# Kernel optimization log

Measured on AMD Instinct MI355X. Metric: run time of the kernel, lower is better.

The kernel has to match this reference:

```python
import jax, jax.numpy as jnp
import numpy as np

N = 50000      # nodes
E = 500000     # edges
F_IN = 128     # num_features
H = 128        # hidden_dim
G = 256        # graphs in batch


def setup_inputs() -> dict:
    key = jax.random.key(0)
    ks = jax.random.split(key, 12)
    x = jax.random.normal(ks[0], (N, F_IN), jnp.float32)
    edge_index = jax.random.randint(ks[1], (2, E), 0, N, dtype=jnp.int32)
    edge_attr = jax.random.uniform(ks[2], (E,), jnp.float32)  # positive edge weights
    batch = jnp.sort(jax.random.randint(ks[3], (N,), 0, G, dtype=jnp.int32))
    s_in = 1.0 / np.sqrt(F_IN)
    s_h = 1.0 / np.sqrt(H)
    return {
        "x": x,
        "edge_index": edge_index,
        "edge_attr": edge_attr,
        "batch": batch,
        "W1": jax.random.normal(ks[4], (H, F_IN), jnp.float32) * s_in,
        "b1": jnp.zeros((H,), jnp.float32),
        "W2": jax.random.normal(ks[5], (H, H), jnp.float32) * s_h,
        "b2": jnp.zeros((H,), jnp.float32),
        "fW1": jax.random.normal(ks[6], (H, H), jnp.float32) * s_h,
        "fb1": jnp.zeros((H,), jnp.float32),
        "fW2": jax.random.normal(ks[7], (1, H), jnp.float32) * s_h,
        "fb2": jnp.zeros((1,), jnp.float32),
    }


def gcn_conv(x, src, dst, ew, W, b, n):
    """PyG GCNConv: linear transform, add self-loops (weight 1),
    symmetric deg^-1/2 normalization with edge weights, scatter-add, bias."""
    h = x @ W.T                                   # [n, H]
    loop = jnp.arange(n, dtype=src.dtype)
    s = jnp.concatenate([src, loop])
    d = jnp.concatenate([dst, loop])
    w = jnp.concatenate([ew, jnp.ones((n,), x.dtype)])
    deg = jax.ops.segment_sum(w, d, num_segments=n)  # weighted in-degree incl. self-loop
    dinv = jnp.where(deg > 0, jax.lax.rsqrt(deg), 0.0)
    norm = dinv[s] * w * dinv[d]                  # [E+n]
    msg = h[s] * norm[:, None]                    # gather + scale: [E+n, H]
    out = jax.ops.segment_sum(msg, d, num_segments=n)  # scatter-add
    return out + b


def reference(x, edge_index, edge_attr, batch, W1, b1, W2, b2, fW1, fb1, fW2, fb2):
    src, dst = edge_index[0], edge_index[1]
    h = jax.nn.relu(gcn_conv(x, src, dst, edge_attr, W1, b1, N))
    h = jax.nn.relu(gcn_conv(h, src, dst, edge_attr, W2, b2, N))
    # global_mean_pool over graph ids
    sums = jax.ops.segment_sum(h, batch, num_segments=G)            # [G, H]
    counts = jax.ops.segment_sum(jnp.ones((N,), h.dtype), batch, num_segments=G)
    pooled = sums / jnp.maximum(counts, 1.0)[:, None]
    o = jax.nn.relu(pooled @ fW1.T + fb1)
    return o @ fW2.T + fb2                                          # [G, 1]
```

## Files before the change

### kernel.cpp

```cpp
#include <hip/hip_runtime.h>
#include <hip/hip_bf16.h>


#define CAP 16
#define NREP 4
#define STRIDE 64

typedef __attribute__((ext_vector_type(8))) short short8;
typedef __attribute__((ext_vector_type(4))) float floatx4;

__device__ inline unsigned short f2bf(float f) {
    unsigned int u = __float_as_uint(f);
    u += 0x7FFF + ((u >> 16) & 1);
    return (unsigned short)(u >> 16);
}
__device__ inline float bf2f(unsigned short h) {
    return __uint_as_float(((unsigned int)h) << 16);
}

__global__ void build_csr(const int* __restrict__ src, const int* __restrict__ dst,
                          const float* __restrict__ ew,
                          int* __restrict__ cnt, int2* __restrict__ csr, int e, int n) {
    int i = blockIdx.x * blockDim.x + threadIdx.x;
    if (i < e) {
        int d = dst[i];
        int r = i & (NREP - 1);
        int pos = atomicAdd(&cnt[(size_t)r * n + d], 1);
        csr[((size_t)d << 6) + (r << 4) + pos] = make_int2(src[i], __float_as_int(ew[i]));
    }
}

__global__ __launch_bounds__(256) void deg_from_csr(const int* __restrict__ cnt,
        const int2* __restrict__ csr, float* __restrict__ dinv, int n) {
    int node = blockIdx.x * 8 + (threadIdx.x >> 5);
    int lane = threadIdx.x & 31;
    float s = 0.0f;
    if (node < n) {
        int pos = lane & 15;
        int sa = lane >> 4;
        int sb = 2 + (lane >> 4);
        int ca = cnt[(size_t)sa * n + node];
        int cb = cnt[(size_t)sb * n + node];
        const int2* b = csr + ((size_t)node << 6);
        if (pos < ca) s += __int_as_float(b[lane].y);
        if (pos < cb) s += __int_as_float(b[32 + lane].y);
    }
#pragma unroll
    for (int off = 16; off > 0; off >>= 1) s += __shfl_down(s, off, 32);
    if (node < n && lane == 0) dinv[node] = rsqrtf(s + 1.0f);
}

__global__ __launch_bounds__(256) void fold_compact(int* __restrict__ cnt,
        int2* __restrict__ csr, const float* __restrict__ dinv, int n) {
    int node = blockIdx.x * 8 + (threadIdx.x >> 5);
    if (node >= n) return;
    int lane = threadIdx.x & 31;
    int c0 = cnt[node];
    int c1 = cnt[(size_t)1 * n + node];
    int c2 = cnt[(size_t)2 * n + node];
    int c3 = cnt[(size_t)3 * n + node];
    int pre[4] = {0, c0, c0 + c1, c0 + c1 + c2};
    int cs[4] = {c0, c1, c2, c3};

    int2* b = csr + ((size_t)node << 6);
    int pos = lane & 15;
    int sa = lane >> 4;
    int sb = 2 + (lane >> 4);
    bool va = pos < cs[sa];
    bool vb = pos < cs[sb];
    int2 ea = va ? b[lane] : make_int2(0, 0);
    int2 eb = vb ? b[32 + lane] : make_int2(0, 0);
    if (va) ea.y = __float_as_int(__int_as_float(ea.y) * dinv[ea.x]);
    if (vb) eb.y = __float_as_int(__int_as_float(eb.y) * dinv[eb.x]);
    if (va) b[pre[sa] + pos] = ea;
    if (vb) b[pre[sb] + pos] = eb;
    if (lane == 0) cnt[node] = c0 + c1 + c2 + c3;
}

#define PW 136
__global__ __launch_bounds__(256) void gemm_f32_nt(const float* __restrict__ X,
        const float* __restrict__ W, unsigned short* __restrict__ C, int M) {
    __shared__ unsigned short whi[128 * PW];
    __shared__ unsigned short wlo[128 * PW];
    const int t = threadIdx.x;

    {
        int j = t >> 1;
        int c0 = (t & 1) * 64;
        const floatx4* wr = (const floatx4*)(W + (size_t)j * 128 + c0);
        unsigned short* dh = &whi[j * PW + c0];
        unsigned short* dl = &wlo[j * PW + c0];
#pragma unroll
        for (int i = 0; i < 16; ++i) {
            floatx4 v = wr[i];
            ushort4 hv, lv;
            hv.x = f2bf(v.x); lv.x = f2bf(v.x - bf2f(hv.x));
            hv.y = f2bf(v.y); lv.y = f2bf(v.y - bf2f(hv.y));
            hv.z = f2bf(v.z); lv.z = f2bf(v.z - bf2f(hv.z));
            hv.w = f2bf(v.w); lv.w = f2bf(v.w - bf2f(hv.w));
            *(ushort4*)(dh + i * 4) = hv;
            *(ushort4*)(dl + i * 4) = lv;
        }
    }
    __syncthreads();

    const int wave = t >> 6;
    const int lane = t & 63;
    const int q = lane >> 4;
    const int ln = lane & 15;
    const int rowbase = blockIdx.x * 128 + wave * 32;

    floatx4 acc[2][8];
#pragma unroll
    for (int s = 0; s < 2; ++s)
#pragma unroll
        for (int ct = 0; ct < 8; ++ct) acc[s][ct] = (floatx4){0.f, 0.f, 0.f, 0.f};

#pragma unroll
    for (int ks = 0; ks < 4; ++ks) {
        short8 ahi[2], alo[2];
#pragma unroll
        for (int s = 0; s < 2; ++s) {
            int row = rowbase + s * 16 + ln;
            int rowc = (row < M) ? row : (M - 1);
            const floatx4* xr = (const floatx4*)(X + (size_t)rowc * 128 + ks * 32 + q * 8);
            floatx4 x0 = xr[0];
            floatx4 x1 = xr[1];
            unsigned short h, l;
            h = f2bf(x0.x); l = f2bf(x0.x - bf2f(h)); ahi[s][0] = (short)h; alo[s][0] = (short)l;
            h = f2bf(x0.y); l = f2bf(x0.y - bf2f(h)); ahi[s][1] = (short)h; alo[s][1] = (short)l;
            h = f2bf(x0.z); l = f2bf(x0.z - bf2f(h)); ahi[s][2] = (short)h; alo[s][2] = (short)l;
            h = f2bf(x0.w); l = f2bf(x0.w - bf2f(h)); ahi[s][3] = (short)h; alo[s][3] = (short)l;
            h = f2bf(x1.x); l = f2bf(x1.x - bf2f(h)); ahi[s][4] = (short)h; alo[s][4] = (short)l;
            h = f2bf(x1.y); l = f2bf(x1.y - bf2f(h)); ahi[s][5] = (short)h; alo[s][5] = (short)l;
            h = f2bf(x1.z); l = f2bf(x1.z - bf2f(h)); ahi[s][6] = (short)h; alo[s][6] = (short)l;
            h = f2bf(x1.w); l = f2bf(x1.w - bf2f(h)); ahi[s][7] = (short)h; alo[s][7] = (short)l;
        }
#pragma unroll
        for (int ct = 0; ct < 8; ++ct) {
            int lidx = (ct * 16 + ln) * PW + ks * 32 + q * 8;
            short8 bhi = *(const short8*)&whi[lidx];
            short8 blo = *(const short8*)&wlo[lidx];
#pragma unroll
            for (int s = 0; s < 2; ++s) {
                acc[s][ct] = __builtin_amdgcn_mfma_f32_16x16x32_bf16(ahi[s], bhi, acc[s][ct], 0, 0, 0);
                acc[s][ct] = __builtin_amdgcn_mfma_f32_16x16x32_bf16(ahi[s], blo, acc[s][ct], 0, 0, 0);
                acc[s][ct] = __builtin_amdgcn_mfma_f32_16x16x32_bf16(alo[s], bhi, acc[s][ct], 0, 0, 0);
            }
        }
    }

#pragma unroll
    for (int s = 0; s < 2; ++s) {
#pragma unroll
        for (int r = 0; r < 4; ++r) {
            int row = rowbase + s * 16 + q * 4 + r;
            if (row < M) {
                unsigned short* cr = C + (size_t)row * 128 + ln;
#pragma unroll
                for (int ct = 0; ct < 8; ++ct) cr[ct * 16] = f2bf(acc[s][ct][r]);
            }
        }
    }
}

__global__ __launch_bounds__(256) void gemm_bf16_nt(const unsigned short* __restrict__ X,
        const float* __restrict__ W, unsigned short* __restrict__ C, int M) {
    __shared__ unsigned short whi[128 * PW];
    __shared__ unsigned short wlo[128 * PW];
    const int t = threadIdx.x;

    {
        int j = t >> 1;
        int c0 = (t & 1) * 64;
        const floatx4* wr = (const floatx4*)(W + (size_t)j * 128 + c0);
        unsigned short* dh = &whi[j * PW + c0];
        unsigned short* dl = &wlo[j * PW + c0];
#pragma unroll
        for (int i = 0; i < 16; ++i) {
            floatx4 v = wr[i];
            ushort4 hv, lv;
            hv.x = f2bf(v.x); lv.x = f2bf(v.x - bf2f(hv.x));
            hv.y = f2bf(v.y); lv.y = f2bf(v.y - bf2f(hv.y));
            hv.z = f2bf(v.z); lv.z = f2bf(v.z - bf2f(hv.z));
            hv.w = f2bf(v.w); lv.w = f2bf(v.w - bf2f(hv.w));
            *(ushort4*)(dh + i * 4) = hv;
            *(ushort4*)(dl + i * 4) = lv;
        }
    }
    __syncthreads();

    const int wave = t >> 6;
    const int lane = t & 63;
    const int q = lane >> 4;
    const int ln = lane & 15;
    const int rowbase = blockIdx.x * 128 + wave * 32;

    floatx4 acc[2][8];
#pragma unroll
    for (int s = 0; s < 2; ++s)
#pragma unroll
        for (int ct = 0; ct < 8; ++ct) acc[s][ct] = (floatx4){0.f, 0.f, 0.f, 0.f};

#pragma unroll
    for (int ks = 0; ks < 4; ++ks) {
        short8 a[2];
#pragma unroll
        for (int s = 0; s < 2; ++s) {
            int row = rowbase + s * 16 + ln;
            int rowc = (row < M) ? row : (M - 1);
            a[s] = *(const short8*)(X + (size_t)rowc * 128 + ks * 32 + q * 8);
        }
#pragma unroll
        for (int ct = 0; ct < 8; ++ct) {
            int lidx = (ct * 16 + ln) * PW + ks * 32 + q * 8;
            short8 bhi = *(const short8*)&whi[lidx];
            short8 blo = *(const short8*)&wlo[lidx];
#pragma unroll
            for (int s = 0; s < 2; ++s) {
                acc[s][ct] = __builtin_amdgcn_mfma_f32_16x16x32_bf16(a[s], bhi, acc[s][ct], 0, 0, 0);
                acc[s][ct] = __builtin_amdgcn_mfma_f32_16x16x32_bf16(a[s], blo, acc[s][ct], 0, 0, 0);
            }
        }
    }

#pragma unroll
    for (int s = 0; s < 2; ++s) {
#pragma unroll
        for (int r = 0; r < 4; ++r) {
            int row = rowbase + s * 16 + q * 4 + r;
            if (row < M) {
                unsigned short* cr = C + (size_t)row * 128 + ln;
#pragma unroll
                for (int ct = 0; ct < 8; ++ct) cr[ct * 16] = f2bf(acc[s][ct][r]);
            }
        }
    }
}

__global__ __launch_bounds__(256) void aggregate_finalize(
        const unsigned short* __restrict__ h, const unsigned short* __restrict__ hlin,
        const int* __restrict__ cnt, const int2* __restrict__ csr,
        const float* __restrict__ dinv, const float* __restrict__ bias,
        unsigned short* __restrict__ outb, int n) {
    int node = blockIdx.x * 8 + (threadIdx.x >> 5);
    if (node >= n) return;
    int lane = threadIdx.x & 31;
    float di = dinv[node];
    float sl = di * di;
    float4 b4 = ((const float4*)bias)[lane];
    ushort4 bse = ((const ushort4*)(hlin + (size_t)node * 128))[lane];
    float4 acc = make_float4(0.f, 0.f, 0.f, 0.f);

    const int2* b = csr + ((size_t)node << 6);
    const int4* bv = (const int4*)b;
    int c = cnt[node];
    int k = 0;
    for (; k + 4 <= c; k += 4) {
        int4 ea = bv[k >> 1];
        int4 eb = bv[(k >> 1) + 1];
        float w0 = __int_as_float(ea.y);
        float w1 = __int_as_float(ea.w);
        float w2 = __int_as_float(eb.y);
        float w3 = __int_as_float(eb.w);
        ushort4 h0 = ((const ushort4*)(h + (size_t)ea.x * 128))[lane];
        ushort4 h1 = ((const ushort4*)(h + (size_t)ea.z * 128))[lane];
        ushort4 h2 = ((const ushort4*)(h + (size_t)eb.x * 128))[lane];
        ushort4 h3 = ((const ushort4*)(h + (size_t)eb.z * 128))[lane];
        acc.x += bf2f(h0.x) * w0 + bf2f(h1.x) * w1 + bf2f(h2.x) * w2 + bf2f(h3.x) * w3;
        acc.y += bf2f(h0.y) * w0 + bf2f(h1.y) * w1 + bf2f(h2.y) * w2 + bf2f(h3.y) * w3;
        acc.z += bf2f(h0.z) * w0 + bf2f(h1.z) * w1 + bf2f(h2.z) * w2 + bf2f(h3.z) * w3;
        acc.w += bf2f(h0.w) * w0 + bf2f(h1.w) * w1 + bf2f(h2.w) * w2 + bf2f(h3.w) * w3;
    }
    if (k + 2 <= c) {
        int4 ea = bv[k >> 1];
        float w0 = __int_as_float(ea.y);
        float w1 = __int_as_float(ea.w);
        ushort4 h0 = ((const ushort4*)(h + (size_t)ea.x * 128))[lane];
        ushort4 h1 = ((const ushort4*)(h + (size_t)ea.z * 128))[lane];
        acc.x += bf2f(h0.x) * w0 + bf2f(h1.x) * w1;
        acc.y += bf2f(h0.y) * w0 + bf2f(h1.y) * w1;
        acc.z += bf2f(h0.z) * w0 + bf2f(h1.z) * w1;
        acc.w += bf2f(h0.w) * w0 + bf2f(h1.w) * w1;
        k += 2;
    }
    if (k < c) {
        int2 ed = b[k];
        float w = __int_as_float(ed.y);
        ushort4 hv = ((const ushort4*)(h + (size_t)ed.x * 128))[lane];
        acc.x += bf2f(hv.x) * w;
        acc.y += bf2f(hv.y) * w;
        acc.z += bf2f(hv.z) * w;
        acc.w += bf2f(hv.w) * w;
    }
    ushort4 o;
    o.x = f2bf(fmaxf(acc.x * di + bf2f(bse.x) * sl + b4.x, 0.0f));
    o.y = f2bf(fmaxf(acc.y * di + bf2f(bse.y) * sl + b4.y, 0.0f));
    o.z = f2bf(fmaxf(acc.z * di + bf2f(bse.z) * sl + b4.z, 0.0f));
    o.w = f2bf(fmaxf(acc.w * di + bf2f(bse.w) * sl + b4.w, 0.0f));
    ((ushort4*)(outb + (size_t)node * 128))[lane] = o;
}

#define POOL_BLOCKS 1024
__global__ __launch_bounds__(128) void pool_partial(const unsigned short* __restrict__ h,
        const int* __restrict__ batch, float* __restrict__ pooled, int n) {
    int chunk = (n + POOL_BLOCKS - 1) / POOL_BLOCKS;
    int s = blockIdx.x * chunk;
    if (s >= n) return;
    int e = min(s + chunk, n);
    int j = threadIdx.x;
    int curg = batch[s];
    float sum = 0.0f;
    for (int i = s; i < e; ++i) {
        int g = batch[i];
        if (g != curg) {
            atomicAdd(&pooled[(size_t)curg * 128 + j], sum);
            sum = 0.0f;
            curg = g;
        }
        sum += bf2f(h[(size_t)i * 128 + j]);
    }
    atomicAdd(&pooled[(size_t)curg * 128 + j], sum);
}

__global__ __launch_bounds__(128) void head_mlp(const float* __restrict__ pooled,
        const int* __restrict__ batch, int n,
        const float* __restrict__ fW1, const float* __restrict__ fb1,
        const float* __restrict__ fW2, const float* __restrict__ fb2,
        float* __restrict__ out) {
    int g = blockIdx.x;
    int j = threadIdx.x;
    int lo = 0, hi = n;
    while (lo < hi) { int mid = (lo + hi) >> 1; if (batch[mid] < g) lo = mid + 1; else hi = mid; }
    int s = lo;
    hi = n;
    while (lo < hi) { int mid = (lo + hi) >> 1; if (batch[mid] < g + 1) lo = mid + 1; else hi = mid; }
    int cnt = lo - s;
    float scale = 1.0f / fmaxf((float)cnt, 1.0f);

    __shared__ float row[128];
    __shared__ float part[2];
    row[j] = pooled[(size_t)g * 128 + j] * scale;
    __syncthreads();
    float acc = fb1[j];
    const float* wr = fW1 + (size_t)j * 128;
#pragma unroll 8
    for (int k = 0; k < 128; ++k) acc += row[k] * wr[k];
    float v = fmaxf(acc, 0.0f) * fW2[j];
#pragma unroll
    for (int off = 32; off > 0; off >>= 1) v += __shfl_down(v, off);
    if ((j & 63) == 0) part[j >> 6] = v;
    __syncthreads();
    if (j == 0) out[g] = part[0] + part[1] + fb2[0];
}

extern "C" void kernel_launch(void* const* d_in, const int* in_sizes, int n_in,
                              void* d_out, int out_size, void* d_ws, size_t ws_size,
                              hipStream_t stream) {
    const float* x   = (const float*)d_in[0];
    const int*   ei  = (const int*)d_in[1];
    const float* ew  = (const float*)d_in[2];
    const int* batch = (const int*)d_in[3];
    const float* W1  = (const float*)d_in[4];
    const float* b1  = (const float*)d_in[5];
    const float* W2  = (const float*)d_in[6];
    const float* b2  = (const float*)d_in[7];
    const float* fW1 = (const float*)d_in[8];
    const float* fb1 = (const float*)d_in[9];
    const float* fW2 = (const float*)d_in[10];
    const float* fb2 = (const float*)d_in[11];
    float* out = (float*)d_out;

    const int N = in_sizes[0] / 128;
    const int E = in_sizes[2];
    const int G = out_size;
    const int* src = ei;
    const int* dst = ei + E;

    unsigned short* A = (unsigned short*)d_ws;
    unsigned short* B = A + (size_t)N * 128;
    int2*  csr  = (int2*)(B + (size_t)N * 128);
    int*   cnt  = (int*)(csr + (size_t)N * STRIDE);
    float* dinv = (float*)(cnt + (size_t)NREP * N);
    float* pooled = dinv + N;

    hipMemsetAsync(cnt, 0, (size_t)NREP * N * sizeof(int), stream);
    build_csr<<<(E + 255) / 256, 256, 0, stream>>>(src, dst, ew, cnt, csr, E, N);
    deg_from_csr<<<(N + 7) / 8, 256, 0, stream>>>(cnt, csr, dinv, N);
    fold_compact<<<(N + 7) / 8, 256, 0, stream>>>(cnt, csr, dinv, N);

    gemm_f32_nt<<<(N + 127) / 128, 256, 0, stream>>>(x, W1, A, N);
    aggregate_finalize<<<(N + 7) / 8, 256, 0, stream>>>(A, A, cnt, csr, dinv, b1, B, N);

    gemm_bf16_nt<<<(N + 127) / 128, 256, 0, stream>>>(B, W2, A, N);
    aggregate_finalize<<<(N + 7) / 8, 256, 0, stream>>>(A, A, cnt, csr, dinv, b2, B, N);

    hipMemsetAsync(pooled, 0, (size_t)G * 128 * sizeof(float), stream);
    pool_partial<<<POOL_BLOCKS, 128, 0, stream>>>(B, batch, pooled, N);
    head_mlp<<<G, 128, 0, stream>>>(pooled, batch, N, fW1, fb1, fW2, fb2, out);
}
```

Baseline: 237.8 us.

## Fuse degree into CSR build, dinv into GEMM, pooling into final aggregate

CSR construction now uses a single per-node counter with a cap of 64 and accumulates weighted degree with float atomics in the same pass. This removes the deg_from_csr and fold_compact kernels. dinv is computed at the start of the first GEMM kernel, and the source-side dinv multiply moves into the aggregation loops as an extra gathered load per edge. The second aggregation is fused with mean-pool partial sums through shared-memory per-block reduction, which drops the bf16 intermediate write, the pool kernel and one memset. The costs are more atomic contention on the single counter, extra dinv gathers, and silent truncation of any node with more than 64 in-edges.

```diff
diff --git a/kernel.cpp b/kernel.cpp
--- a/kernel.cpp
+++ b/kernel.cpp
@@ -2,9 +2,7 @@
 #include <hip/hip_bf16.h>
 
 
-#define CAP 16
-#define NREP 4
-#define STRIDE 64
+#define CAP 64
 
 typedef __attribute__((ext_vector_type(8))) short short8;
 typedef __attribute__((ext_vector_type(4))) float floatx4;
@@ -20,66 +18,28 @@
 
 __global__ void build_csr(const int* __restrict__ src, const int* __restrict__ dst,
                           const float* __restrict__ ew,
-                          int* __restrict__ cnt, int2* __restrict__ csr, int e, int n) {
+                          int* __restrict__ cnt, float* __restrict__ deg,
+                          int2* __restrict__ csr, int e, int n) {
     int i = blockIdx.x * blockDim.x + threadIdx.x;
     if (i < e) {
         int d = dst[i];
-        int r = i & (NREP - 1);
-        int pos = atomicAdd(&cnt[(size_t)r * n + d], 1);
-        csr[((size_t)d << 6) + (r << 4) + pos] = make_int2(src[i], __float_as_int(ew[i]));
-    }
-}
-
-__global__ __launch_bounds__(256) void deg_from_csr(const int* __restrict__ cnt,
-        const int2* __restrict__ csr, float* __restrict__ dinv, int n) {
-    int node = blockIdx.x * 8 + (threadIdx.x >> 5);
-    int lane = threadIdx.x & 31;
-    float s = 0.0f;
-    if (node < n) {
-        int pos = lane & 15;
-        int sa = lane >> 4;
-        int sb = 2 + (lane >> 4);
-        int ca = cnt[(size_t)sa * n + node];
-        int cb = cnt[(size_t)sb * n + node];
-        const int2* b = csr + ((size_t)node << 6);
-        if (pos < ca) s += __int_as_float(b[lane].y);
-        if (pos < cb) s += __int_as_float(b[32 + lane].y);
-    }
-#pragma unroll
-    for (int off = 16; off > 0; off >>= 1) s += __shfl_down(s, off, 32);
-    if (node < n && lane == 0) dinv[node] = rsqrtf(s + 1.0f);
-}
-
-__global__ __launch_bounds__(256) void fold_compact(int* __restrict__ cnt,
-        int2* __restrict__ csr, const float* __restrict__ dinv, int n) {
-    int node = blockIdx.x * 8 + (threadIdx.x >> 5);
-    if (node >= n) return;
-    int lane = threadIdx.x & 31;
-    int c0 = cnt[node];
-    int c1 = cnt[(size_t)1 * n + node];
-    int c2 = cnt[(size_t)2 * n + node];
-    int c3 = cnt[(size_t)3 * n + node];
-    int pre[4] = {0, c0, c0 + c1, c0 + c1 + c2};
-    int cs[4] = {c0, c1, c2, c3};
-
-    int2* b = csr + ((size_t)node << 6);
-    int pos = lane & 15;
-    int sa = lane >> 4;
-    int sb = 2 + (lane >> 4);
-    bool va = pos < cs[sa];
-    bool vb = pos < cs[sb];
-    int2 ea = va ? b[lane] : make_int2(0, 0);
-    int2 eb = vb ? b[32 + lane] : make_int2(0, 0);
-    if (va) ea.y = __float_as_int(__int_as_float(ea.y) * dinv[ea.x]);
-    if (vb) eb.y = __float_as_int(__int_as_float(eb.y) * dinv[eb.x]);
-    if (va) b[pre[sa] + pos] = ea;
-    if (vb) b[pre[sb] + pos] = eb;
-    if (lane == 0) cnt[node] = c0 + c1 + c2 + c3;
+        float w = ew[i];
+        int pos = atomicAdd(&cnt[d], 1);
+        if (pos < CAP)
+            csr[((size_t)d << 6) + pos] = make_int2(src[i], __float_as_int(w));
+        atomicAdd(&deg[d], w);
+    }
 }
 
 #define PW 136
 __global__ __launch_bounds__(256) void gemm_f32_nt(const float* __restrict__ X,
-        const float* __restrict__ W, unsigned short* __restrict__ C, int M) {
+        const float* __restrict__ W, unsigned short* __restrict__ C,
+        const float* __restrict__ deg, float* __restrict__ dinv, int M) {
+    {
+        int gid = blockIdx.x * 256 + threadIdx.x;
+        if (gid < M) dinv[gid] = rsqrtf(deg[gid] + 1.0f);
+    }
+
     __shared__ unsigned short whi[128 * PW];
     __shared__ unsigned short wlo[128 * PW];
     const int t = threadIdx.x;
@@ -255,14 +215,15 @@
     const int2* b = csr + ((size_t)node << 6);
     const int4* bv = (const int4*)b;
     int c = cnt[node];
+    if (c > CAP) c = CAP;
     int k = 0;
     for (; k + 4 <= c; k += 4) {
         int4 ea = bv[k >> 1];
         int4 eb = bv[(k >> 1) + 1];
-        float w0 = __int_as_float(ea.y);
-        float w1 = __int_as_float(ea.w);
-        float w2 = __int_as_float(eb.y);
-        float w3 = __int_as_float(eb.w);
+        float w0 = __int_as_float(ea.y) * dinv[ea.x];
+        float w1 = __int_as_float(ea.w) * dinv[ea.z];
+        float w2 = __int_as_float(eb.y) * dinv[eb.x];
+        float w3 = __int_as_float(eb.w) * dinv[eb.z];
         ushort4 h0 = ((const ushort4*)(h + (size_t)ea.x * 128))[lane];
         ushort4 h1 = ((const ushort4*)(h + (size_t)ea.z * 128))[lane];
         ushort4 h2 = ((const ushort4*)(h + (size_t)eb.x * 128))[lane];
@@ -274,8 +235,8 @@
     }
     if (k + 2 <= c) {
         int4 ea = bv[k >> 1];
-        float w0 = __int_as_float(ea.y);
-        float w1 = __int_as_float(ea.w);
+        float w0 = __int_as_float(ea.y) * dinv[ea.x];
+        float w1 = __int_as_float(ea.w) * dinv[ea.z];
         ushort4 h0 = ((const ushort4*)(h + (size_t)ea.x * 128))[lane];
         ushort4 h1 = ((const ushort4*)(h + (size_t)ea.z * 128))[lane];
         acc.x += bf2f(h0.x) * w0 + bf2f(h1.x) * w1;
@@ -286,7 +247,7 @@
     }
     if (k < c) {
         int2 ed = b[k];
-        float w = __int_as_float(ed.y);
+        float w = __int_as_float(ed.y) * dinv[ed.x];
         ushort4 hv = ((const ushort4*)(h + (size_t)ed.x * 128))[lane];
         acc.x += bf2f(hv.x) * w;
         acc.y += bf2f(hv.y) * w;
@@ -301,26 +262,94 @@
     ((ushort4*)(outb + (size_t)node * 128))[lane] = o;
 }
 
-#define POOL_BLOCKS 1024
-__global__ __launch_bounds__(128) void pool_partial(const unsigned short* __restrict__ h,
+__global__ __launch_bounds__(256) void aggregate_pool(
+        const unsigned short* __restrict__ h,
+        const int* __restrict__ cnt, const int2* __restrict__ csr,
+        const float* __restrict__ dinv, const float* __restrict__ bias,
         const int* __restrict__ batch, float* __restrict__ pooled, int n) {
-    int chunk = (n + POOL_BLOCKS - 1) / POOL_BLOCKS;
-    int s = blockIdx.x * chunk;
-    if (s >= n) return;
-    int e = min(s + chunk, n);
-    int j = threadIdx.x;
-    int curg = batch[s];
-    float sum = 0.0f;
-    for (int i = s; i < e; ++i) {
-        int g = batch[i];
-        if (g != curg) {
-            atomicAdd(&pooled[(size_t)curg * 128 + j], sum);
-            sum = 0.0f;
-            curg = g;
-        }
-        sum += bf2f(h[(size_t)i * 128 + j]);
-    }
-    atomicAdd(&pooled[(size_t)curg * 128 + j], sum);
+    int slot = threadIdx.x >> 5;
+    int node = blockIdx.x * 8 + slot;
+    int lane = threadIdx.x & 31;
+    __shared__ float red[8][128];
+    __shared__ int grp[8];
+
+    float4 o = make_float4(0.f, 0.f, 0.f, 0.f);
+    int g = -1;
+    if (node < n) {
+        g = batch[node];
+        float di = dinv[node];
+        float sl = di * di;
+        float4 b4 = ((const float4*)bias)[lane];
+        ushort4 bse = ((const ushort4*)(h + (size_t)node * 128))[lane];
+        float4 acc = make_float4(0.f, 0.f, 0.f, 0.f);
+
+        const int2* b = csr + ((size_t)node << 6);
+        const int4* bv = (const int4*)b;
+        int c = cnt[node];
+        if (c > CAP) c = CAP;
+        int k = 0;
+        for (; k + 4 <= c; k += 4) {
+            int4 ea = bv[k >> 1];
+            int4 eb = bv[(k >> 1) + 1];
+            float w0 = __int_as_float(ea.y) * dinv[ea.x];
+            float w1 = __int_as_float(ea.w) * dinv[ea.z];
+            float w2 = __int_as_float(eb.y) * dinv[eb.x];
+            float w3 = __int_as_float(eb.w) * dinv[eb.z];
+            ushort4 h0 = ((const ushort4*)(h + (size_t)ea.x * 128))[lane];
+            ushort4 h1 = ((const ushort4*)(h + (size_t)ea.z * 128))[lane];
+            ushort4 h2 = ((const ushort4*)(h + (size_t)eb.x * 128))[lane];
+            ushort4 h3 = ((const ushort4*)(h + (size_t)eb.z * 128))[lane];
+            acc.x += bf2f(h0.x) * w0 + bf2f(h1.x) * w1 + bf2f(h2.x) * w2 + bf2f(h3.x) * w3;
+            acc.y += bf2f(h0.y) * w0 + bf2f(h1.y) * w1 + bf2f(h2.y) * w2 + bf2f(h3.y) * w3;
+            acc.z += bf2f(h0.z) * w0 + bf2f(h1.z) * w1 + bf2f(h2.z) * w2 + bf2f(h3.z) * w3;
+            acc.w += bf2f(h0.w) * w0 + bf2f(h1.w) * w1 + bf2f(h2.w) * w2 + bf2f(h3.w) * w3;
+        }
+        if (k + 2 <= c) {
+            int4 ea = bv[k >> 1];
+            float w0 = __int_as_float(ea.y) * dinv[ea.x];
+            float w1 = __int_as_float(ea.w) * dinv[ea.z];
+            ushort4 h0 = ((const ushort4*)(h + (size_t)ea.x * 128))[lane];
+            ushort4 h1 = ((const ushort4*)(h + (size_t)ea.z * 128))[lane];
+            acc.x += bf2f(h0.x) * w0 + bf2f(h1.x) * w1;
+            acc.y += bf2f(h0.y) * w0 + bf2f(h1.y) * w1;
+            acc.z += bf2f(h0.z) * w0 + bf2f(h1.z) * w1;
+            acc.w += bf2f(h0.w) * w0 + bf2f(h1.w) * w1;
+            k += 2;
+        }
+        if (k < c) {
+            int2 ed = b[k];
+            float w = __int_as_float(ed.y) * dinv[ed.x];
+            ushort4 hv = ((const ushort4*)(h + (size_t)ed.x * 128))[lane];
+            acc.x += bf2f(hv.x) * w;
+            acc.y += bf2f(hv.y) * w;
+            acc.z += bf2f(hv.z) * w;
+            acc.w += bf2f(hv.w) * w;
+        }
+        o.x = fmaxf(acc.x * di + bf2f(bse.x) * sl + b4.x, 0.0f);
+        o.y = fmaxf(acc.y * di + bf2f(bse.y) * sl + b4.y, 0.0f);
+        o.z = fmaxf(acc.z * di + bf2f(bse.z) * sl + b4.z, 0.0f);
+        o.w = fmaxf(acc.w * di + bf2f(bse.w) * sl + b4.w, 0.0f);
+    }
+    if (lane == 0) grp[slot] = g;
+    *(float4*)&red[slot][lane * 4] = o;
+    __syncthreads();
+
+    if (threadIdx.x < 128) {
+        int j = threadIdx.x;
+        float s = 0.f;
+        int cg = -1;
+#pragma unroll
+        for (int r = 0; r < 8; ++r) {
+            int gr = grp[r];
+            if (gr != cg) {
+                if (cg >= 0) atomicAdd(&pooled[(size_t)cg * 128 + j], s);
+                s = 0.f;
+                cg = gr;
+            }
+            if (gr >= 0) s += red[r][j];
+        }
+        if (cg >= 0) atomicAdd(&pooled[(size_t)cg * 128 + j], s);
+    }
 }
 
 __global__ __launch_bounds__(128) void head_mlp(const float* __restrict__ pooled,
@@ -380,22 +409,19 @@
     unsigned short* A = (unsigned short*)d_ws;
     unsigned short* B = A + (size_t)N * 128;
     int2*  csr  = (int2*)(B + (size_t)N * 128);
-    int*   cnt  = (int*)(csr + (size_t)N * STRIDE);
-    float* dinv = (float*)(cnt + (size_t)NREP * N);
-    float* pooled = dinv + N;
-
-    hipMemsetAsync(cnt, 0, (size_t)NREP * N * sizeof(int), stream);
-    build_csr<<<(E + 255) / 256, 256, 0, stream>>>(src, dst, ew, cnt, csr, E, N);
-    deg_from_csr<<<(N + 7) / 8, 256, 0, stream>>>(cnt, csr, dinv, N);
-    fold_compact<<<(N + 7) / 8, 256, 0, stream>>>(cnt, csr, dinv, N);
-
-    gemm_f32_nt<<<(N + 127) / 128, 256, 0, stream>>>(x, W1, A, N);
+    int*   cnt  = (int*)(csr + (size_t)N * CAP);
+    float* deg  = (float*)(cnt + N);
+    float* pooled = deg + N;
+    float* dinv = pooled + (size_t)G * 128;
+
+    hipMemsetAsync(cnt, 0, ((size_t)2 * N + (size_t)G * 128) * sizeof(int), stream);
+    build_csr<<<(E + 255) / 256, 256, 0, stream>>>(src, dst, ew, cnt, deg, csr, E, N);
+
+    gemm_f32_nt<<<(N + 127) / 128, 256, 0, stream>>>(x, W1, A, deg, dinv, N);
     aggregate_finalize<<<(N + 7) / 8, 256, 0, stream>>>(A, A, cnt, csr, dinv, b1, B, N);
 
     gemm_bf16_nt<<<(N + 127) / 128, 256, 0, stream>>>(B, W2, A, N);
-    aggregate_finalize<<<(N + 7) / 8, 256, 0, stream>>>(A, A, cnt, csr, dinv, b2, B, N);
-
-    hipMemsetAsync(pooled, 0, (size_t)G * 128 * sizeof(float), stream);
-    pool_partial<<<POOL_BLOCKS, 128, 0, stream>>>(B, batch, pooled, N);
+    aggregate_pool<<<(N + 7) / 8, 256, 0, stream>>>(A, cnt, csr, dinv, b2, batch, pooled, N);
+
     head_mlp<<<G, 128, 0, stream>>>(pooled, batch, N, fW1, fb1, fW2, fb2, out);
 }
```

Result: faster. 226.8 us (-4.6%).
